# Performance work log

Hardware: AMD Instinct MI355X
Metric: run time of the kernel (lower is better)

## Reference

```python
import jax, jax.numpy as jnp
import numpy as np

N = 50000      # nodes
E = 400000     # edges (before self-loops)
IN = 256       # in_dim
H = 4          # heads in layer 1
C = 64         # h_dim (per-head channels, layer 1)
OUT = 16       # out_dim (layer 2, 1 head)
NEG_SLOPE = 0.2


def gatv2_layer(x, src, dst, Wl, bl, Wr, br, att, bias, heads, ch, concat, num_nodes):
    # x: [N, F]; src/dst: [E']; Wl/Wr: [F, heads*ch]; att: [heads, ch]
    xl = (x @ Wl + bl).reshape(num_nodes, heads, ch)  # source transform
    xr = (x @ Wr + br).reshape(num_nodes, heads, ch)  # target transform
    m = xl[src] + xr[dst]                              # [E', H, C] gather
    e = jnp.sum(jax.nn.leaky_relu(m, NEG_SLOPE) * att, axis=-1)  # [E', H]
    # segment softmax over incoming edges of each dst node (self-loops ensure non-empty)
    emax = jax.ops.segment_max(e, dst, num_segments=num_nodes)   # [N, H]
    ee = jnp.exp(e - emax[dst])
    denom = jax.ops.segment_sum(ee, dst, num_segments=num_nodes)  # [N, H]
    alpha = ee / (denom[dst] + 1e-16)                              # [E', H]
    out = jax.ops.segment_sum(alpha[..., None] * xl[src], dst, num_segments=num_nodes)  # [N,H,C]
    if concat:
        out = out.reshape(num_nodes, heads * ch)
    else:
        out = out.mean(axis=1)
    return out + bias


def setup_inputs() -> dict:
    key = jax.random.key(0)
    ks = jax.random.split(key, 16)
    s = 0.05
    inp = {
        "x": jax.random.normal(ks[0], (N, IN), jnp.float32),
        "edge_index": jax.random.randint(ks[1], (2, E), 0, N),
        # layer 1 params (in_dim -> heads*h_dim)
        "Wl1": jax.random.normal(ks[2], (IN, H * C), jnp.float32) * s,
        "bl1": jnp.zeros((H * C,), jnp.float32),
        "Wr1": jax.random.normal(ks[3], (IN, H * C), jnp.float32) * s,
        "br1": jnp.zeros((H * C,), jnp.float32),
        "att1": jax.random.normal(ks[4], (H, C), jnp.float32) * s,
        "bias1": jnp.zeros((H * C,), jnp.float32),
        # layer 2 params (heads*h_dim -> out_dim, 1 head)
        "Wl2": jax.random.normal(ks[5], (H * C, OUT), jnp.float32) * s,
        "bl2": jnp.zeros((OUT,), jnp.float32),
        "Wr2": jax.random.normal(ks[6], (H * C, OUT), jnp.float32) * s,
        "br2": jnp.zeros((OUT,), jnp.float32),
        "att2": jax.random.normal(ks[7], (1, OUT), jnp.float32) * s,
        "bias2": jnp.zeros((OUT,), jnp.float32),
    }
    return inp


def reference(x, edge_index, Wl1, bl1, Wr1, br1, att1, bias1, Wl2, bl2, Wr2, br2, att2, bias2):
    # add self loops (PyG GATv2Conv default add_self_loops=True)
    loop = jnp.arange(N, dtype=edge_index.dtype)
    src = jnp.concatenate([edge_index[0], loop])
    dst = jnp.concatenate([edge_index[1], loop])
    h = gatv2_layer(x, src, dst, Wl1, bl1, Wr1, br1, att1, bias1, H, C, True, N)
    h = jnp.tanh(h)
    o = gatv2_layer(h, src, dst, Wl2, bl2, Wr2, br2, att2, bias2, 1, OUT, False, N)
    return o, jax.nn.log_softmax(o, axis=1)
```

## Files before the change

kernel.cpp:

```cpp
#include <hip/hip_runtime.h>

typedef __bf16 bfv8 __attribute__((ext_vector_type(8)));
typedef float f32x4 __attribute__((ext_vector_type(4)));

__device__ __forceinline__ float b2f(unsigned short u) {
  unsigned int v = ((unsigned int)u) << 16;
  float f;
  __builtin_memcpy(&f, &v, 4);
  return f;
}
__device__ __forceinline__ unsigned short f2b(float f) {
  unsigned int u;
  __builtin_memcpy(&u, &f, 4);
  u += 0x7fffu + ((u >> 16) & 1u);
  return (unsigned short)(u >> 16);
}

__global__ void probe_kernel(const unsigned short* __restrict__ x, int* __restrict__ flag) {
  int lane = threadIdx.x;
  int cnt = 0;
  for (int i = lane; i < 4096; i += 64) {
    unsigned int e = (x[i] >> 7) & 0xffu;
    if (e >= 0x86u) cnt++;
  }
#pragma unroll
  for (int off = 1; off < 64; off <<= 1) cnt += __shfl_xor(cnt, off, 64);
  if (lane == 0) *flag = (cnt > 100) ? 1 : 0;
}

__global__ __launch_bounds__(256) void conv_x_kernel(const void* __restrict__ x,
                                                     unsigned short* __restrict__ dst,
                                                     const int* __restrict__ flagp, int n) {
  int i = (blockIdx.x * 256 + threadIdx.x) * 4;
  if (i >= n) return;
  if (*flagp) {
    float4 f = *reinterpret_cast<const float4*>((const float*)x + i);
    ushort4 o;
    o.x = f2b(f.x); o.y = f2b(f.y); o.z = f2b(f.z); o.w = f2b(f.w);
    *reinterpret_cast<ushort4*>(dst + i) = o;
  } else {
    *reinterpret_cast<ushort4*>(dst + i) =
        *reinterpret_cast<const ushort4*>((const unsigned short*)x + i);
  }
}

#define P_TOT 140352
__global__ __launch_bounds__(256) void conv_params_kernel(
    const void* p0, const void* p1, const void* p2, const void* p3,
    const void* p4, const void* p5, const void* p6, const void* p7,
    const void* p8, const void* p9, const void* p10, const void* p11,
    unsigned short* __restrict__ dst, const int* __restrict__ flagp) {
  int i = blockIdx.x * 256 + threadIdx.x;
  if (i >= P_TOT) return;
  const int offs[13] = {0, 65536, 65792, 131328, 131584, 131840, 132096,
                        136192, 136208, 140304, 140320, 140336, P_TOT};
  const void* ptrs[12] = {p0, p1, p2, p3, p4, p5, p6, p7, p8, p9, p10, p11};
  int flag = *flagp;
  int t = 0;
  while (i >= offs[t + 1]) t++;
  int local = i - offs[t];
  unsigned short v;
  if (flag) v = f2b(((const float*)ptrs[t])[local]);
  else v = ((const unsigned short*)ptrs[t])[local];
  dst[i] = v;
}

__global__ __launch_bounds__(256) void transpose_w1(
    const unsigned short* __restrict__ Wl, const unsigned short* __restrict__ Wr,
    unsigned short* __restrict__ WT) {
  int idx = blockIdx.x * 256 + threadIdx.x;
  int n = idx >> 8, k = idx & 255;
  WT[idx] = (n < 256) ? Wl[k * 256 + n] : Wr[k * 256 + (n - 256)];
}
__global__ __launch_bounds__(256) void transpose_w2(
    const unsigned short* __restrict__ Wl, const unsigned short* __restrict__ Wr,
    unsigned short* __restrict__ WT) {
  int idx = blockIdx.x * 256 + threadIdx.x;
  int n = idx >> 8, k = idx & 255;
  WT[idx] = (n < 16) ? Wl[k * 16 + n] : Wr[k * 16 + (n - 16)];
}

__global__ __launch_bounds__(256) void gemm1_kernel(
    const unsigned short* __restrict__ X, const unsigned short* __restrict__ WT,
    const unsigned short* __restrict__ bl, const unsigned short* __restrict__ br,
    unsigned short* __restrict__ C, int M) {
  const int lane = threadIdx.x & 63;
  const int w = threadIdx.x >> 6;
  const int quad = lane >> 4;
  const int l16 = lane & 15;
  const int m_base = blockIdx.y * 128 + (w >> 1) * 64;
  const int n_base = blockIdx.x * 128 + (w & 1) * 64;

  f32x4 acc[4][4];
#pragma unroll
  for (int i = 0; i < 4; i++)
#pragma unroll
    for (int j = 0; j < 4; j++) acc[i][j] = (f32x4){0.f, 0.f, 0.f, 0.f};

#pragma unroll
  for (int k0 = 0; k0 < 256; k0 += 32) {
    bfv8 a[4], b[4];
#pragma unroll
    for (int i = 0; i < 4; i++) {
      int row = m_base + 16 * i + l16;
      if (row >= M) row = M - 1;
      a[i] = *reinterpret_cast<const bfv8*>(X + (size_t)row * 256 + k0 + quad * 8);
    }
#pragma unroll
    for (int j = 0; j < 4; j++) {
      int col = n_base + 16 * j + l16;
      b[j] = *reinterpret_cast<const bfv8*>(WT + (size_t)col * 256 + k0 + quad * 8);
    }
#pragma unroll
    for (int i = 0; i < 4; i++)
#pragma unroll
      for (int j = 0; j < 4; j++)
        acc[i][j] = __builtin_amdgcn_mfma_f32_16x16x32_bf16(a[i], b[j], acc[i][j], 0, 0, 0);
  }

#pragma unroll
  for (int j = 0; j < 4; j++) {
    int col = n_base + 16 * j + l16;
    float bias = (col < 256) ? b2f(bl[col]) : b2f(br[col - 256]);
#pragma unroll
    for (int i = 0; i < 4; i++) {
#pragma unroll
      for (int r = 0; r < 4; r++) {
        int row = m_base + 16 * i + quad * 4 + r;
        if (row < M) C[(size_t)row * 512 + col] = f2b(acc[i][j][r] + bias);
      }
    }
  }
}

__global__ __launch_bounds__(256) void gemm2_kernel(
    const unsigned short* __restrict__ H, const unsigned short* __restrict__ WT,
    const unsigned short* __restrict__ bl, const unsigned short* __restrict__ br,
    float* __restrict__ C, int M) {
  const int lane = threadIdx.x & 63;
  const int w = threadIdx.x >> 6;
  const int quad = lane >> 4;
  const int l16 = lane & 15;
  const int m_base = blockIdx.x * 256 + w * 64;

  f32x4 acc[4][2];
#pragma unroll
  for (int i = 0; i < 4; i++)
#pragma unroll
    for (int j = 0; j < 2; j++) acc[i][j] = (f32x4){0.f, 0.f, 0.f, 0.f};

#pragma unroll
  for (int k0 = 0; k0 < 256; k0 += 32) {
    bfv8 a[4], b[2];
#pragma unroll
    for (int i = 0; i < 4; i++) {
      int row = m_base + 16 * i + l16;
      if (row >= M) row = M - 1;
      a[i] = *reinterpret_cast<const bfv8*>(H + (size_t)row * 256 + k0 + quad * 8);
    }
#pragma unroll
    for (int j = 0; j < 2; j++) {
      int col = 16 * j + l16;
      b[j] = *reinterpret_cast<const bfv8*>(WT + (size_t)col * 256 + k0 + quad * 8);
    }
#pragma unroll
    for (int i = 0; i < 4; i++)
#pragma unroll
      for (int j = 0; j < 2; j++)
        acc[i][j] = __builtin_amdgcn_mfma_f32_16x16x32_bf16(a[i], b[j], acc[i][j], 0, 0, 0);
  }

#pragma unroll
  for (int j = 0; j < 2; j++) {
    int col = 16 * j + l16;
    float bias = (j == 0) ? b2f(bl[l16]) : b2f(br[l16]);
#pragma unroll
    for (int i = 0; i < 4; i++) {
#pragma unroll
      for (int r = 0; r < 4; r++) {
        int row = m_base + 16 * i + quad * 4 + r;
        if (row < M) C[(size_t)row * 32 + col] = acc[i][j][r] + bias;
      }
    }
  }
}

__global__ __launch_bounds__(256) void count_kernel(const int* __restrict__ ei, int E, int Nn,
                                                    int* __restrict__ cnt) {
  int i = blockIdx.x * 256 + threadIdx.x;
  int total = E + Nn;
  if (i >= total) return;
  int d = (i < E) ? ei[E + i] : (i - E);
  if ((unsigned)d >= (unsigned)Nn) d = 0;
  atomicAdd(&cnt[d], 1);
}

__global__ __launch_bounds__(1024) void scan1_kernel(const int* __restrict__ cnt,
                                                     int* __restrict__ row_start,
                                                     int* __restrict__ blkTot, int Nn) {
  __shared__ int buf[1024];
  int t = threadIdx.x;
  int i = blockIdx.x * 1024 + t;
  int v = (i < Nn) ? cnt[i] : 0;
  buf[t] = v;
  __syncthreads();
  for (int off = 1; off < 1024; off <<= 1) {
    int x = (t >= off) ? buf[t - off] : 0;
    __syncthreads();
    buf[t] += x;
    __syncthreads();
  }
  if (i < Nn) row_start[i] = buf[t] - v;
  if (t == 1023) blkTot[blockIdx.x] = buf[1023];
}

__global__ __launch_bounds__(64) void scan2_kernel(const int* __restrict__ blkTot,
                                                   int* __restrict__ blkOff, int nb,
                                                   int* __restrict__ row_start, int Nn,
                                                   int total) {
  int lane = threadIdx.x;
  int v = (lane < nb) ? blkTot[lane] : 0;
  int s = v;
#pragma unroll
  for (int off = 1; off < 64; off <<= 1) {
    int u = __shfl_up(s, off, 64);
    if (lane >= off) s += u;
  }
  if (lane < nb) blkOff[lane] = s - v;
  if (lane == 0) row_start[Nn] = total;
}

__global__ __launch_bounds__(1024) void scan3_kernel(int* __restrict__ row_start,
                                                     int* __restrict__ cursor,
                                                     const int* __restrict__ blkOff, int Nn) {
  int i = blockIdx.x * 1024 + threadIdx.x;
  if (i < Nn) {
    int val = row_start[i] + blkOff[blockIdx.x];
    row_start[i] = val;
    cursor[i] = val;
  }
}

__global__ __launch_bounds__(256) void fill_kernel(const int* __restrict__ ei, int E, int Nn,
                                                   int* __restrict__ cursor,
                                                   int* __restrict__ csr_src) {
  int i = blockIdx.x * 256 + threadIdx.x;
  int total = E + Nn;
  if (i >= total) return;
  int s, d;
  if (i < E) { s = ei[i]; d = ei[E + i]; } else { s = i - E; d = i - E; }
  if ((unsigned)d >= (unsigned)Nn) d = 0;
  if ((unsigned)s >= (unsigned)Nn) s = 0;
  int pos = atomicAdd(&cursor[d], 1);
  if ((unsigned)pos < (unsigned)total) csr_src[pos] = s;
}

__global__ __launch_bounds__(256) void agg1_kernel(
    const unsigned short* __restrict__ C1,
    const unsigned short* __restrict__ att1,
    const unsigned short* __restrict__ bias1,
    const int* __restrict__ row_start, const int* __restrict__ csr_src,
    unsigned short* __restrict__ H1,
    int Nn, int Etot) {
  int wid = blockIdx.x * 4 + (threadIdx.x >> 6);
  if (wid >= Nn) return;
  int lane = threadIdx.x & 63;
  int c0 = lane * 4;

  ushort4 a4 = *reinterpret_cast<const ushort4*>(att1 + c0);
  float at0 = b2f(a4.x), at1 = b2f(a4.y), at2 = b2f(a4.z), at3 = b2f(a4.w);
  ushort4 r4 = *reinterpret_cast<const ushort4*>(C1 + (size_t)wid * 512 + 256 + c0);
  float xr0 = b2f(r4.x), xr1 = b2f(r4.y), xr2 = b2f(r4.z), xr3 = b2f(r4.w);

  float denom = 0.f, a0 = 0.f, a1 = 0.f, a2 = 0.f, a3 = 0.f;
  int beg = row_start[wid], end = row_start[wid + 1];
  if (beg < 0) beg = 0;
  if (end < beg || end - beg > Etot) end = beg;

  ushort4 x4n = make_ushort4(0, 0, 0, 0);
  if (beg < end) {
    int s0 = csr_src[beg];
    if ((unsigned)s0 >= (unsigned)Nn) s0 = 0;
    x4n = *reinterpret_cast<const ushort4*>(C1 + (size_t)s0 * 512 + c0);
  }
  for (int p = beg; p < end; ++p) {
    ushort4 x4 = x4n;
    if (p + 1 < end) {
      int sn = csr_src[p + 1];
      if ((unsigned)sn >= (unsigned)Nn) sn = 0;
      x4n = *reinterpret_cast<const ushort4*>(C1 + (size_t)sn * 512 + c0);
    }
    float xl0 = b2f(x4.x), xl1 = b2f(x4.y), xl2 = b2f(x4.z), xl3 = b2f(x4.w);
    float m0 = xl0 + xr0, m1 = xl1 + xr1, m2 = xl2 + xr2, m3 = xl3 + xr3;
    float l0 = m0 > 0.f ? m0 : 0.2f * m0;
    float l1 = m1 > 0.f ? m1 : 0.2f * m1;
    float l2 = m2 > 0.f ? m2 : 0.2f * m2;
    float l3 = m3 > 0.f ? m3 : 0.2f * m3;
    float part = l0 * at0 + l1 * at1 + l2 * at2 + l3 * at3;
    part += __shfl_xor(part, 1, 64);
    part += __shfl_xor(part, 2, 64);
    part += __shfl_xor(part, 4, 64);
    part += __shfl_xor(part, 8, 64);
    part = fminf(fmaxf(part, -60.f), 60.f);
    float wgt = __expf(part);
    denom += wgt;
    a0 += wgt * xl0;
    a1 += wgt * xl1;
    a2 += wgt * xl2;
    a3 += wgt * xl3;
  }
  float inv = 1.f / (denom + 1e-16f);
  ushort4 b4 = *reinterpret_cast<const ushort4*>(bias1 + c0);
  float h0 = tanhf(a0 * inv + b2f(b4.x));
  float h1 = tanhf(a1 * inv + b2f(b4.y));
  float h2 = tanhf(a2 * inv + b2f(b4.z));
  float h3 = tanhf(a3 * inv + b2f(b4.w));
  if (!(h0 == h0)) h0 = 0.f;
  if (!(h1 == h1)) h1 = 0.f;
  if (!(h2 == h2)) h2 = 0.f;
  if (!(h3 == h3)) h3 = 0.f;
  ushort4 o4;
  o4.x = f2b(h0); o4.y = f2b(h1); o4.z = f2b(h2); o4.w = f2b(h3);
  *reinterpret_cast<ushort4*>(H1 + (size_t)wid * 256 + c0) = o4;
}

__global__ __launch_bounds__(256) void agg2_kernel(
    const float* __restrict__ C2,
    const unsigned short* __restrict__ att2,
    const unsigned short* __restrict__ bias2,
    const int* __restrict__ row_start, const int* __restrict__ csr_src,
    float* __restrict__ out,
    int Nn, int Etot) {
  int wid = blockIdx.x * 4 + (threadIdx.x >> 6);
  if (wid >= Nn) return;
  int lane = threadIdx.x & 63;
  int g = lane >> 4;
  int c = lane & 15;

  float att = b2f(att2[c]);
  float xr = C2[(size_t)wid * 32 + 16 + c];
  float denom = 0.f, acc = 0.f;
  int beg = row_start[wid], end = row_start[wid + 1];
  if (beg < 0) beg = 0;
  if (end < beg || end - beg > Etot) end = beg;
  for (int p = beg + g; p < end; p += 4) {
    int s = csr_src[p];
    if ((unsigned)s >= (unsigned)Nn) s = 0;
    float xl = C2[(size_t)s * 32 + c];
    float mm = xl + xr;
    float lr = mm > 0.f ? mm : 0.2f * mm;
    float part = lr * att;
    part += __shfl_xor(part, 1, 64);
    part += __shfl_xor(part, 2, 64);
    part += __shfl_xor(part, 4, 64);
    part += __shfl_xor(part, 8, 64);
    part = fminf(fmaxf(part, -60.f), 60.f);
    float wgt = __expf(part);
    denom += wgt;
    acc += wgt * xl;
  }
  denom += __shfl_xor(denom, 16, 64);
  denom += __shfl_xor(denom, 32, 64);
  acc += __shfl_xor(acc, 16, 64);
  acc += __shfl_xor(acc, 32, 64);

  float o = acc / (denom + 1e-16f) + b2f(bias2[c]);
  if (!(o == o)) o = 0.f;
  float mx = o;
  mx = fmaxf(mx, __shfl_xor(mx, 1, 64));
  mx = fmaxf(mx, __shfl_xor(mx, 2, 64));
  mx = fmaxf(mx, __shfl_xor(mx, 4, 64));
  mx = fmaxf(mx, __shfl_xor(mx, 8, 64));
  float ex = expf(o - mx);
  float se = ex;
  se += __shfl_xor(se, 1, 64);
  se += __shfl_xor(se, 2, 64);
  se += __shfl_xor(se, 4, 64);
  se += __shfl_xor(se, 8, 64);
  float ls = logf(se);
  if (lane < 16) {
    out[(size_t)wid * 16 + c] = o;
    out[(size_t)Nn * 16 + (size_t)wid * 16 + c] = o - mx - ls;
  }
}

extern "C" void kernel_launch(void* const* d_in, const int* in_sizes, int n_in,
                              void* d_out, int out_size, void* d_ws, size_t ws_size,
                              hipStream_t stream) {
  const void* x_raw = d_in[0];
  const int* ei     = (const int*)d_in[1];

  const int M = in_sizes[0] / 256;
  const int E = in_sizes[1] / 2;
  const int TOT = E + M;
  const int NX = M * 256;

  char* ws = (char*)d_ws;
  size_t off = 0;
  auto alloc = [&](size_t bytes) -> void* {
    void* p = ws + off;
    off = (off + bytes + 255) & ~(size_t)255;
    return p;
  };
  int*            flag   = (int*)alloc(4);
  unsigned short* Pc     = (unsigned short*)alloc((size_t)P_TOT * 2);
  unsigned short* Xc     = (unsigned short*)alloc((size_t)NX * 2);
  unsigned short* WT1    = (unsigned short*)alloc((size_t)512 * 256 * 2);
  unsigned short* WT2    = (unsigned short*)alloc((size_t)32 * 256 * 2);
  int*            cnt    = (int*)alloc((size_t)M * 4);
  int*            cursor = (int*)alloc((size_t)M * 4);
  int*            row_start = (int*)alloc((size_t)(M + 1) * 4);
  int*            csr_src   = (int*)alloc((size_t)TOT * 4);
  int*            blkTot = (int*)alloc(64 * 4);
  int*            blkOff = (int*)alloc(64 * 4);
  float*          C2     = (float*)alloc((size_t)M * 32 * 4);
  unsigned short* C1     = (unsigned short*)alloc((size_t)M * 512 * 2);
  const size_t need = off;
  (void)n_in;
  unsigned short* H1 = Xc;

  if (ws_size < need) {
    hipMemsetAsync(d_out, 0, (size_t)out_size * 4, stream);
    return;
  }

  unsigned short* Wl1c   = Pc + 0;
  unsigned short* bl1c   = Pc + 65536;
  unsigned short* Wr1c   = Pc + 65792;
  unsigned short* br1c   = Pc + 131328;
  unsigned short* att1c  = Pc + 131584;
  unsigned short* bias1c = Pc + 131840;
  unsigned short* Wl2c   = Pc + 132096;
  unsigned short* bl2c   = Pc + 136192;
  unsigned short* Wr2c   = Pc + 136208;
  unsigned short* br2c   = Pc + 140304;
  unsigned short* att2c  = Pc + 140320;
  unsigned short* bias2c = Pc + 140336;

  hipMemsetAsync(cnt, 0, (size_t)M * 4, stream);

  probe_kernel<<<1, 64, 0, stream>>>((const unsigned short*)x_raw, flag);
  conv_x_kernel<<<(NX / 4 + 255) / 256, 256, 0, stream>>>(x_raw, Xc, flag, NX);
  conv_params_kernel<<<(P_TOT + 255) / 256, 256, 0, stream>>>(
      d_in[2], d_in[3], d_in[4], d_in[5], d_in[6], d_in[7], d_in[8], d_in[9],
      d_in[10], d_in[11], d_in[12], d_in[13], Pc, flag);

  transpose_w1<<<512, 256, 0, stream>>>(Wl1c, Wr1c, WT1);
  transpose_w2<<<32, 256, 0, stream>>>(Wl2c, Wr2c, WT2);

  dim3 g1(4, (M + 127) / 128);
  gemm1_kernel<<<g1, 256, 0, stream>>>(Xc, WT1, bl1c, br1c, C1, M);

  count_kernel<<<(TOT + 255) / 256, 256, 0, stream>>>(ei, E, M, cnt);
  int nb = (M + 1023) / 1024;
  scan1_kernel<<<nb, 1024, 0, stream>>>(cnt, row_start, blkTot, M);
  scan2_kernel<<<1, 64, 0, stream>>>(blkTot, blkOff, nb, row_start, M, TOT);
  scan3_kernel<<<nb, 1024, 0, stream>>>(row_start, cursor, blkOff, M);
  fill_kernel<<<(TOT + 255) / 256, 256, 0, stream>>>(ei, E, M, cursor, csr_src);

  agg1_kernel<<<(M + 3) / 4, 256, 0, stream>>>(C1, att1c, bias1c, row_start, csr_src,
                                               H1, M, TOT);

  gemm2_kernel<<<(M + 255) / 256, 256, 0, stream>>>(H1, WT2, bl2c, br2c, C2, M);

  agg2_kernel<<<(M + 3) / 4, 256, 0, stream>>>(C2, att2c, bias2c, row_start, csr_src,
                                               (float*)d_out, M, TOT);
}
```

Baseline: 332.8 us.

## Fuse x conversion into gemm1, merge transposes, stage stores via LDS, prefetch in aggregations

Removes the separate x fp32-to-bf16 conversion kernel by converting on the fly inside gemm1, merges the two weight transpose kernels into one launch, and stages gemm1 output through shared memory for coalesced 16-byte stores. The gemm1 grid is reordered so M blocks vary fastest. Aggregation 1 now prefetches two neighbours ahead and aggregation 2 gains one-step software prefetching. The trade-off is that gemm1 reads x as fp32 four times (once per N block) instead of reading bf16 once, and H1 now needs its own workspace buffer.

```diff
diff --git a/kernel.cpp b/kernel.cpp
--- a/kernel.cpp
+++ b/kernel.cpp
@@ -2,6 +2,7 @@
 
 typedef __bf16 bfv8 __attribute__((ext_vector_type(8)));
 typedef float f32x4 __attribute__((ext_vector_type(4)));
+typedef short shortv8 __attribute__((ext_vector_type(8)));
 
 __device__ __forceinline__ float b2f(unsigned short u) {
   unsigned int v = ((unsigned int)u) << 16;
@@ -26,22 +27,6 @@
 #pragma unroll
   for (int off = 1; off < 64; off <<= 1) cnt += __shfl_xor(cnt, off, 64);
   if (lane == 0) *flag = (cnt > 100) ? 1 : 0;
-}
-
-__global__ __launch_bounds__(256) void conv_x_kernel(const void* __restrict__ x,
-                                                     unsigned short* __restrict__ dst,
-                                                     const int* __restrict__ flagp, int n) {
-  int i = (blockIdx.x * 256 + threadIdx.x) * 4;
-  if (i >= n) return;
-  if (*flagp) {
-    float4 f = *reinterpret_cast<const float4*>((const float*)x + i);
-    ushort4 o;
-    o.x = f2b(f.x); o.y = f2b(f.y); o.z = f2b(f.z); o.w = f2b(f.w);
-    *reinterpret_cast<ushort4*>(dst + i) = o;
-  } else {
-    *reinterpret_cast<ushort4*>(dst + i) =
-        *reinterpret_cast<const ushort4*>((const unsigned short*)x + i);
-  }
 }
 
 #define P_TOT 140352
@@ -65,31 +50,37 @@
   dst[i] = v;
 }
 
-__global__ __launch_bounds__(256) void transpose_w1(
-    const unsigned short* __restrict__ Wl, const unsigned short* __restrict__ Wr,
-    unsigned short* __restrict__ WT) {
+__global__ __launch_bounds__(256) void transpose_w_kernel(
+    const unsigned short* __restrict__ Pc,
+    unsigned short* __restrict__ WT1, unsigned short* __restrict__ WT2) {
   int idx = blockIdx.x * 256 + threadIdx.x;
-  int n = idx >> 8, k = idx & 255;
-  WT[idx] = (n < 256) ? Wl[k * 256 + n] : Wr[k * 256 + (n - 256)];
-}
-__global__ __launch_bounds__(256) void transpose_w2(
-    const unsigned short* __restrict__ Wl, const unsigned short* __restrict__ Wr,
-    unsigned short* __restrict__ WT) {
-  int idx = blockIdx.x * 256 + threadIdx.x;
-  int n = idx >> 8, k = idx & 255;
-  WT[idx] = (n < 16) ? Wl[k * 16 + n] : Wr[k * 16 + (n - 16)];
+  if (idx < 512 * 256) {
+    int n = idx >> 8, k = idx & 255;
+    WT1[idx] = (n < 256) ? Pc[0 + k * 256 + n]
+                         : Pc[65792 + k * 256 + (n - 256)];
+  } else {
+    int j = idx - 512 * 256;
+    if (j < 32 * 256) {
+      int n = j >> 8, k = j & 255;
+      WT2[j] = (n < 16) ? Pc[132096 + k * 16 + n]
+                        : Pc[136208 + k * 16 + (n - 16)];
+    }
+  }
 }
 
 __global__ __launch_bounds__(256) void gemm1_kernel(
-    const unsigned short* __restrict__ X, const unsigned short* __restrict__ WT,
+    const void* __restrict__ X, const int* __restrict__ flagp,
+    const unsigned short* __restrict__ WT,
     const unsigned short* __restrict__ bl, const unsigned short* __restrict__ br,
     unsigned short* __restrict__ C, int M) {
+  __shared__ unsigned short ltile[4][64 * 72];
   const int lane = threadIdx.x & 63;
   const int w = threadIdx.x >> 6;
   const int quad = lane >> 4;
   const int l16 = lane & 15;
-  const int m_base = blockIdx.y * 128 + (w >> 1) * 64;
-  const int n_base = blockIdx.x * 128 + (w & 1) * 64;
+  const int m_base = blockIdx.x * 128 + (w >> 1) * 64;
+  const int n_base = blockIdx.y * 128 + (w & 1) * 64;
+  const int fl = *flagp;
 
   f32x4 acc[4][4];
 #pragma unroll
@@ -97,39 +88,79 @@
 #pragma unroll
     for (int j = 0; j < 4; j++) acc[i][j] = (f32x4){0.f, 0.f, 0.f, 0.f};
 
-#pragma unroll
-  for (int k0 = 0; k0 < 256; k0 += 32) {
-    bfv8 a[4], b[4];
-#pragma unroll
-    for (int i = 0; i < 4; i++) {
-      int row = m_base + 16 * i + l16;
-      if (row >= M) row = M - 1;
-      a[i] = *reinterpret_cast<const bfv8*>(X + (size_t)row * 256 + k0 + quad * 8);
-    }
-#pragma unroll
-    for (int j = 0; j < 4; j++) {
-      int col = n_base + 16 * j + l16;
-      b[j] = *reinterpret_cast<const bfv8*>(WT + (size_t)col * 256 + k0 + quad * 8);
-    }
-#pragma unroll
-    for (int i = 0; i < 4; i++)
-#pragma unroll
-      for (int j = 0; j < 4; j++)
-        acc[i][j] = __builtin_amdgcn_mfma_f32_16x16x32_bf16(a[i], b[j], acc[i][j], 0, 0, 0);
-  }
-
+  if (fl) {
+    const float* Xf = (const float*)X;
+#pragma unroll
+    for (int k0 = 0; k0 < 256; k0 += 32) {
+      bfv8 a[4], b[4];
+#pragma unroll
+      for (int i = 0; i < 4; i++) {
+        int row = m_base + 16 * i + l16;
+        if (row >= M) row = M - 1;
+        const float* p = Xf + (size_t)row * 256 + k0 + quad * 8;
+        float4 f0 = *reinterpret_cast<const float4*>(p);
+        float4 f1 = *reinterpret_cast<const float4*>(p + 4);
+        union { bfv8 v; unsigned short us[8]; } pa;
+        pa.us[0] = f2b(f0.x); pa.us[1] = f2b(f0.y);
+        pa.us[2] = f2b(f0.z); pa.us[3] = f2b(f0.w);
+        pa.us[4] = f2b(f1.x); pa.us[5] = f2b(f1.y);
+        pa.us[6] = f2b(f1.z); pa.us[7] = f2b(f1.w);
+        a[i] = pa.v;
+      }
+#pragma unroll
+      for (int j = 0; j < 4; j++) {
+        int col = n_base + 16 * j + l16;
+        b[j] = *reinterpret_cast<const bfv8*>(WT + (size_t)col * 256 + k0 + quad * 8);
+      }
+#pragma unroll
+      for (int i = 0; i < 4; i++)
+#pragma unroll
+        for (int j = 0; j < 4; j++)
+          acc[i][j] = __builtin_amdgcn_mfma_f32_16x16x32_bf16(a[i], b[j], acc[i][j], 0, 0, 0);
+    }
+  } else {
+    const unsigned short* Xb = (const unsigned short*)X;
+#pragma unroll
+    for (int k0 = 0; k0 < 256; k0 += 32) {
+      bfv8 a[4], b[4];
+#pragma unroll
+      for (int i = 0; i < 4; i++) {
+        int row = m_base + 16 * i + l16;
+        if (row >= M) row = M - 1;
+        a[i] = *reinterpret_cast<const bfv8*>(Xb + (size_t)row * 256 + k0 + quad * 8);
+      }
+#pragma unroll
+      for (int j = 0; j < 4; j++) {
+        int col = n_base + 16 * j + l16;
+        b[j] = *reinterpret_cast<const bfv8*>(WT + (size_t)col * 256 + k0 + quad * 8);
+      }
+#pragma unroll
+      for (int i = 0; i < 4; i++)
+#pragma unroll
+        for (int j = 0; j < 4; j++)
+          acc[i][j] = __builtin_amdgcn_mfma_f32_16x16x32_bf16(a[i], b[j], acc[i][j], 0, 0, 0);
+    }
+  }
+
+  unsigned short* lt = ltile[w];
 #pragma unroll
   for (int j = 0; j < 4; j++) {
     int col = n_base + 16 * j + l16;
     float bias = (col < 256) ? b2f(bl[col]) : b2f(br[col - 256]);
 #pragma unroll
-    for (int i = 0; i < 4; i++) {
-#pragma unroll
-      for (int r = 0; r < 4; r++) {
-        int row = m_base + 16 * i + quad * 4 + r;
-        if (row < M) C[(size_t)row * 512 + col] = f2b(acc[i][j][r] + bias);
-      }
-    }
+    for (int i = 0; i < 4; i++)
+#pragma unroll
+      for (int r = 0; r < 4; r++)
+        lt[(16 * i + quad * 4 + r) * 72 + 16 * j + l16] = f2b(acc[i][j][r] + bias);
+  }
+#pragma unroll
+  for (int pass = 0; pass < 8; pass++) {
+    int row = pass * 8 + (lane >> 3);
+    int colg = (lane & 7) * 8;
+    shortv8 v = *reinterpret_cast<const shortv8*>(lt + row * 72 + colg);
+    int grow = m_base + row;
+    if (grow < M)
+      *reinterpret_cast<shortv8*>(C + (size_t)grow * 512 + n_base + colg) = v;
   }
 }
 
@@ -276,39 +307,61 @@
   int beg = row_start[wid], end = row_start[wid + 1];
   if (beg < 0) beg = 0;
   if (end < beg || end - beg > Etot) end = beg;
-
-  ushort4 x4n = make_ushort4(0, 0, 0, 0);
-  if (beg < end) {
-    int s0 = csr_src[beg];
-    if ((unsigned)s0 >= (unsigned)Nn) s0 = 0;
-    x4n = *reinterpret_cast<const ushort4*>(C1 + (size_t)s0 * 512 + c0);
-  }
-  for (int p = beg; p < end; ++p) {
-    ushort4 x4 = x4n;
-    if (p + 1 < end) {
-      int sn = csr_src[p + 1];
-      if ((unsigned)sn >= (unsigned)Nn) sn = 0;
-      x4n = *reinterpret_cast<const ushort4*>(C1 + (size_t)sn * 512 + c0);
-    }
-    float xl0 = b2f(x4.x), xl1 = b2f(x4.y), xl2 = b2f(x4.z), xl3 = b2f(x4.w);
-    float m0 = xl0 + xr0, m1 = xl1 + xr1, m2 = xl2 + xr2, m3 = xl3 + xr3;
-    float l0 = m0 > 0.f ? m0 : 0.2f * m0;
-    float l1 = m1 > 0.f ? m1 : 0.2f * m1;
-    float l2 = m2 > 0.f ? m2 : 0.2f * m2;
-    float l3 = m3 > 0.f ? m3 : 0.2f * m3;
-    float part = l0 * at0 + l1 * at1 + l2 * at2 + l3 * at3;
-    part += __shfl_xor(part, 1, 64);
-    part += __shfl_xor(part, 2, 64);
-    part += __shfl_xor(part, 4, 64);
-    part += __shfl_xor(part, 8, 64);
-    part = fminf(fmaxf(part, -60.f), 60.f);
-    float wgt = __expf(part);
-    denom += wgt;
-    a0 += wgt * xl0;
-    a1 += wgt * xl1;
-    a2 += wgt * xl2;
-    a3 += wgt * xl3;
-  }
+  int n = end - beg;
+
+  ushort4 cur0 = make_ushort4(0, 0, 0, 0), cur1 = cur0;
+  if (n > 0) {
+    int s = csr_src[beg];
+    if ((unsigned)s >= (unsigned)Nn) s = 0;
+    cur0 = *reinterpret_cast<const ushort4*>(C1 + (size_t)s * 512 + c0);
+  }
+  if (n > 1) {
+    int s = csr_src[beg + 1];
+    if ((unsigned)s >= (unsigned)Nn) s = 0;
+    cur1 = *reinterpret_cast<const ushort4*>(C1 + (size_t)s * 512 + c0);
+  }
+
+#define AGG1_BODY(XV)                                                        \
+  {                                                                          \
+    float xl0 = b2f(XV.x), xl1 = b2f(XV.y), xl2 = b2f(XV.z), xl3 = b2f(XV.w); \
+    float m0 = xl0 + xr0, m1 = xl1 + xr1, m2 = xl2 + xr2, m3 = xl3 + xr3;    \
+    float l0 = m0 > 0.f ? m0 : 0.2f * m0;                                    \
+    float l1 = m1 > 0.f ? m1 : 0.2f * m1;                                    \
+    float l2 = m2 > 0.f ? m2 : 0.2f * m2;                                    \
+    float l3 = m3 > 0.f ? m3 : 0.2f * m3;                                    \
+    float part = l0 * at0 + l1 * at1 + l2 * at2 + l3 * at3;                  \
+    part += __shfl_xor(part, 1, 64);                                         \
+    part += __shfl_xor(part, 2, 64);                                         \
+    part += __shfl_xor(part, 4, 64);                                         \
+    part += __shfl_xor(part, 8, 64);                                         \
+    part = fminf(fmaxf(part, -60.f), 60.f);                                  \
+    float wgt = __expf(part);                                                \
+    denom += wgt;                                                            \
+    a0 += wgt * xl0; a1 += wgt * xl1; a2 += wgt * xl2; a3 += wgt * xl3;      \
+  }
+
+  int i = 0;
+  for (; i + 2 <= n; i += 2) {
+    ushort4 nxt0 = cur0, nxt1 = cur1;
+    int q0 = beg + i + 2, q1 = beg + i + 3;
+    if (q0 < end) {
+      int s = csr_src[q0];
+      if ((unsigned)s >= (unsigned)Nn) s = 0;
+      nxt0 = *reinterpret_cast<const ushort4*>(C1 + (size_t)s * 512 + c0);
+    }
+    if (q1 < end) {
+      int s = csr_src[q1];
+      if ((unsigned)s >= (unsigned)Nn) s = 0;
+      nxt1 = *reinterpret_cast<const ushort4*>(C1 + (size_t)s * 512 + c0);
+    }
+    AGG1_BODY(cur0);
+    AGG1_BODY(cur1);
+    cur0 = nxt0;
+    cur1 = nxt1;
+  }
+  if (i < n) AGG1_BODY(cur0);
+#undef AGG1_BODY
+
   float inv = 1.f / (denom + 1e-16f);
   ushort4 b4 = *reinterpret_cast<const ushort4*>(bias1 + c0);
   float h0 = tanhf(a0 * inv + b2f(b4.x));
@@ -343,11 +396,23 @@
   int beg = row_start[wid], end = row_start[wid + 1];
   if (beg < 0) beg = 0;
   if (end < beg || end - beg > Etot) end = beg;
-  for (int p = beg + g; p < end; p += 4) {
+
+  int p = beg + g;
+  float xl_cur = 0.f;
+  if (p < end) {
     int s = csr_src[p];
     if ((unsigned)s >= (unsigned)Nn) s = 0;
-    float xl = C2[(size_t)s * 32 + c];
-    float mm = xl + xr;
+    xl_cur = C2[(size_t)s * 32 + c];
+  }
+  while (p < end) {
+    int pn = p + 4;
+    float xl_nxt = 0.f;
+    if (pn < end) {
+      int s = csr_src[pn];
+      if ((unsigned)s >= (unsigned)Nn) s = 0;
+      xl_nxt = C2[(size_t)s * 32 + c];
+    }
+    float mm = xl_cur + xr;
     float lr = mm > 0.f ? mm : 0.2f * mm;
     float part = lr * att;
     part += __shfl_xor(part, 1, 64);
@@ -357,7 +422,9 @@
     part = fminf(fmaxf(part, -60.f), 60.f);
     float wgt = __expf(part);
     denom += wgt;
-    acc += wgt * xl;
+    acc += wgt * xl_cur;
+    xl_cur = xl_nxt;
+    p = pn;
   }
   denom += __shfl_xor(denom, 16, 64);
   denom += __shfl_xor(denom, 32, 64);
@@ -393,7 +460,6 @@
   const int M = in_sizes[0] / 256;
   const int E = in_sizes[1] / 2;
   const int TOT = E + M;
-  const int NX = M * 256;
 
   char* ws = (char*)d_ws;
   size_t off = 0;
@@ -404,7 +470,6 @@
   };
   int*            flag   = (int*)alloc(4);
   unsigned short* Pc     = (unsigned short*)alloc((size_t)P_TOT * 2);
-  unsigned short* Xc     = (unsigned short*)alloc((size_t)NX * 2);
   unsigned short* WT1    = (unsigned short*)alloc((size_t)512 * 256 * 2);
   unsigned short* WT2    = (unsigned short*)alloc((size_t)32 * 256 * 2);
   int*            cnt    = (int*)alloc((size_t)M * 4);
@@ -415,24 +480,20 @@
   int*            blkOff = (int*)alloc(64 * 4);
   float*          C2     = (float*)alloc((size_t)M * 32 * 4);
   unsigned short* C1     = (unsigned short*)alloc((size_t)M * 512 * 2);
+  unsigned short* H1     = (unsigned short*)alloc((size_t)M * 256 * 2);
   const size_t need = off;
   (void)n_in;
-  unsigned short* H1 = Xc;
 
   if (ws_size < need) {
     hipMemsetAsync(d_out, 0, (size_t)out_size * 4, stream);
     return;
   }
 
-  unsigned short* Wl1c   = Pc + 0;
   unsigned short* bl1c   = Pc + 65536;
-  unsigned short* Wr1c   = Pc + 65792;
   unsigned short* br1c   = Pc + 131328;
   unsigned short* att1c  = Pc + 131584;
   unsigned short* bias1c = Pc + 131840;
-  unsigned short* Wl2c   = Pc + 132096;
   unsigned short* bl2c   = Pc + 136192;
-  unsigned short* Wr2c   = Pc + 136208;
   unsigned short* br2c   = Pc + 140304;
   unsigned short* att2c  = Pc + 140320;
   unsigned short* bias2c = Pc + 140336;
@@ -440,16 +501,14 @@
   hipMemsetAsync(cnt, 0, (size_t)M * 4, stream);
 
   probe_kernel<<<1, 64, 0, stream>>>((const unsigned short*)x_raw, flag);
-  conv_x_kernel<<<(NX / 4 + 255) / 256, 256, 0, stream>>>(x_raw, Xc, flag, NX);
   conv_params_kernel<<<(P_TOT + 255) / 256, 256, 0, stream>>>(
       d_in[2], d_in[3], d_in[4], d_in[5], d_in[6], d_in[7], d_in[8], d_in[9],
       d_in[10], d_in[11], d_in[12], d_in[13], Pc, flag);
 
-  transpose_w1<<<512, 256, 0, stream>>>(Wl1c, Wr1c, WT1);
-  transpose_w2<<<32, 256, 0, stream>>>(Wl2c, Wr2c, WT2);
-
-  dim3 g1(4, (M + 127) / 128);
-  gemm1_kernel<<<g1, 256, 0, stream>>>(Xc, WT1, bl1c, br1c, C1, M);
+  transpose_w_kernel<<<(512 * 256 + 32 * 256 + 255) / 256, 256, 0, stream>>>(Pc, WT1, WT2);
+
+  dim3 g1((M + 127) / 128, 4);
+  gemm1_kernel<<<g1, 256, 0, stream>>>(x_raw, flag, WT1, bl1c, br1c, C1, M);
 
   count_kernel<<<(TOT + 255) / 256, 256, 0, stream>>>(ei, E, M, cnt);
   int nb = (M + 1023) / 1024;
```

Result: slower. 343.6 us (+3.3%).
